# Kernel optimization log

Hardware: AMD Instinct MI355X
Metric: run time of the kernel (lower is better)

Reference implementation:

```python
import jax, jax.numpy as jnp
import numpy as np

N = 100000      # nodes
IN_DIM = 128    # input feature dim
HID = 64        # hidden_dim / out_dim per head
HEADS = 4
E_RAND = 1600000  # random edges; self-loops appended -> E = E_RAND + N
SCALES = 3


def setup_inputs() -> dict:
    key = jax.random.key(0)
    ks = jax.random.split(key, 12)
    h = jax.random.normal(ks[0], (N, IN_DIM), dtype=jnp.float32)
    src = jax.random.randint(ks[1], (E_RAND,), 0, N)
    dst = jax.random.randint(ks[2], (E_RAND,), 0, N)
    loop = jnp.arange(N)
    src = jnp.concatenate([src, loop])  # self-loops ensure every dst has a mailbox
    dst = jnp.concatenate([dst, loop])
    frac_cover_mat = jax.random.randint(ks[3], (N, SCALES), 0, N)
    # learned params (bias=False everywhere); xavier-ish scaling
    layer1_fc = jax.random.normal(ks[4], (HEADS, HID, IN_DIM), jnp.float32) / np.sqrt(IN_DIM)
    layer1_attn = jax.random.normal(ks[5], (HEADS, 2 * HID), jnp.float32) * 0.1
    layer2_fc = jax.random.normal(ks[6], (HID, HID * HEADS), jnp.float32) / np.sqrt(HID * HEADS)
    layer2_attn = jax.random.normal(ks[7], (2 * HID,), jnp.float32) * 0.1
    frac_w = jax.random.normal(ks[8], (SCALES, HID, IN_DIM), jnp.float32) / np.sqrt(IN_DIM)
    frac_final_w = jax.random.normal(ks[9], (HID, SCALES * HID), jnp.float32) / np.sqrt(SCALES * HID)
    fc2_w = jax.random.normal(ks[10], (HID, 2 * HID), jnp.float32) / np.sqrt(2 * HID)
    return {"h": h, "src": src, "dst": dst, "frac_cover_mat": frac_cover_mat,
            "layer1_fc": layer1_fc, "layer1_attn": layer1_attn,
            "layer2_fc": layer2_fc, "layer2_attn": layer2_attn,
            "frac_w": frac_w, "frac_final_w": frac_final_w, "fc2_w": fc2_w}


def _gat_layer(z, src, dst, attn_w, n):
    # attn(cat([z_src, z_dst])) == z_src @ a_src + z_dst @ a_dst  (bias-free Linear)
    d = z.shape[1]
    e = jax.nn.leaky_relu(z[src] @ attn_w[:d] + z[dst] @ attn_w[d:])  # [E]
    # segment softmax over incoming edges of each dst node
    m = jax.ops.segment_max(e, dst, num_segments=n)
    ex = jnp.exp(e - m[dst])
    denom = jax.ops.segment_sum(ex, dst, num_segments=n)
    alpha = ex / denom[dst]                                   # [E]
    return jax.ops.segment_sum(alpha[:, None] * z[src], dst, num_segments=n)  # [N, d]


def reference(h, src, dst, frac_cover_mat,
              layer1_fc, layer1_attn, layer2_fc, layer2_attn,
              frac_w, frac_final_w, fc2_w):
    n = h.shape[0]
    # layer1: multi-head GAT, merge='cat'
    heads = []
    for i in range(layer1_fc.shape[0]):
        z = h @ layer1_fc[i].T                                # [N, HID]
        heads.append(_gat_layer(z, src, dst, layer1_attn[i], n))
    h_nei = jax.nn.elu(jnp.concatenate(heads, axis=1))        # [N, HID*HEADS]
    # layer2: single-head GAT
    z2 = h_nei @ layer2_fc.T                                  # [N, HID]
    h_nei = _gat_layer(z2, src, dst, layer2_attn, n)          # [N, HID]
    # fractal layer (dropout = identity in eval)
    h_all = [h[frac_cover_mat[:, s]] @ frac_w[s].T for s in range(frac_w.shape[0])]
    h_frac = jnp.concatenate(h_all, axis=1) @ frac_final_w.T  # [N, HID]
    # fc2 on cat([h_nei, h_frac]); dropout identity
    h_global = jnp.concatenate([h_nei, h_frac], axis=1) @ fc2_w.T  # [N, HID]
    # AvgPooling over single graph -> [1, HID]
    return jnp.mean(h_global, axis=0, keepdims=True)
```

## Files before the change

kernel.cpp:

```cpp
#include <hip/hip_runtime.h>
#include <math.h>


#define CAP 128

typedef unsigned int  uint_t;
typedef unsigned short ushort_t;
typedef __attribute__((ext_vector_type(8))) short short8;
typedef __attribute__((ext_vector_type(4))) float floatx4;
typedef __attribute__((ext_vector_type(2))) float floatx2;

__device__ __forceinline__ float wred_sum(float v){
#pragma unroll
  for (int o = 1; o < 64; o <<= 1) v += __shfl_xor(v, o, 64);
  return v;
}
__device__ __forceinline__ float lrelu(float x){ return x >= 0.f ? x : 0.01f*x; }
__device__ __forceinline__ ushort_t f2b(float f){
  uint_t u = __float_as_uint(f);
  u = (u + 0x7FFFu + ((u >> 16) & 1u)) >> 16;
  return (ushort_t)u;
}
__device__ __forceinline__ float b2f_lo(uint_t w){ return __uint_as_float(w << 16); }
__device__ __forceinline__ float b2f_hi(uint_t w){ return __uint_as_float(w & 0xFFFF0000u); }

__device__ __forceinline__ void agg8(uint2 u, float4 al,
    floatx2& c00, floatx2& c01, floatx2& c10, floatx2& c11){
  floatx2 p0 = __builtin_amdgcn_cvt_pk_f32_fp8(u.x, false);
  floatx2 p1 = __builtin_amdgcn_cvt_pk_f32_fp8(u.x, true);
  floatx2 p2 = __builtin_amdgcn_cvt_pk_f32_fp8(u.y, false);
  floatx2 p3 = __builtin_amdgcn_cvt_pk_f32_fp8(u.y, true);
  floatx2 aXY = {al.x, al.y}, aZW = {al.z, al.w};
  c00 += aXY * p0;
  c01 += aZW * p1;
  c10 += aXY * p2;
  c11 += aZW * p3;
}

__global__ void k_prep(const float* __restrict__ W1, const float* __restrict__ W2,
                       const float* __restrict__ a1, const float* __restrict__ a2,
                       const int* __restrict__ dstI, int E,
                       const int* __restrict__ fcm, int N3, int* __restrict__ cnt,
                       ushort_t* __restrict__ w1bp, float* __restrict__ v2,
                       int* __restrict__ deg){
  __shared__ float v[8][128];
  const int bx = blockIdx.x, t = threadIdx.x;
  if (bx < 128){
    int idx = bx*256 + t;
    int j = idx & 7, lane = (idx >> 3) & 63, ks = (idx >> 9) & 3, tt = idx >> 11;
    int n = tt*16 + (lane & 15), k = ks*32 + (lane >> 4)*8 + j;
    int hh = tt >> 2, m = tt & 3;
    int pt = (m < 2) ? (hh*2 + m) : (8 + hh*2 + (m - 2));
    w1bp[((pt*4 + ks)*64 + lane)*8 + j] = f2b(W1[n*128 + k]);
  } else if (bx == 128){
    for (int o = t; o < 1024; o += 256){
      int col = o >> 7, k = o & 127, hh = col & 3, off = (col >> 2)*64;
      float s = 0.f;
      for (int n = 0; n < 64; n++) s += a1[hh*128 + off + n] * W1[(hh*64 + n)*128 + k];
      v[col][k] = s;
    }
    __syncthreads();
    for (int idx = t; idx < 2048; idx += 256){
      int j = idx & 7, lane = (idx >> 3) & 63, ks = idx >> 9;
      int col = lane & 15, k = ks*32 + (lane >> 4)*8 + j;
      w1bp[32768 + idx] = (col < 8) ? f2b(v[col][k]) : (ushort_t)0;
    }
  } else if (bx == 129){
    float s0 = 0.f, s1 = 0.f;
    for (int j = 0; j < 64; j++){
      float wjk = W2[j*256 + t];
      s0 += wjk * a2[j];
      s1 += wjk * a2[64 + j];
    }
    v2[t] = s0; v2[256 + t] = s1;
  } else {
    const int nb = gridDim.x - 130;
    for (int i = (bx-130)*256 + t; i < E; i += nb*256)
      atomicAdd(&deg[dstI[i]], 1);
    for (int i = (bx-130)*256 + t; i < N3; i += nb*256){
      int v3 = fcm[i];
      atomicAdd(&cnt[v3*3 + (i % 3)], 1);
    }
  }
}

__global__ __launch_bounds__(256) void k_scan1(const int* __restrict__ deg, int* __restrict__ part){
  __shared__ int tmp[256];
  int t = threadIdx.x;
  tmp[t] = deg[blockIdx.x*256 + t];
  __syncthreads();
  for (int off = 128; off > 0; off >>= 1){
    if (t < off) tmp[t] += tmp[t+off];
    __syncthreads();
  }
  if (t == 0) part[blockIdx.x] = tmp[0];
}
__global__ __launch_bounds__(512) void k_scan2(int* __restrict__ part, int B){
  __shared__ int tmp[512];
  int t = threadIdx.x;
  int v = (t < B) ? part[t] : 0;
  tmp[t] = v; __syncthreads();
  for (int off = 1; off < 512; off <<= 1){
    int x = (t >= off) ? tmp[t-off] : 0;
    __syncthreads();
    tmp[t] += x;
    __syncthreads();
  }
  if (t < B) part[t] = tmp[t] - v;
}
__global__ __launch_bounds__(256) void k_scan3(const int* __restrict__ deg, const int* __restrict__ part,
    int* __restrict__ rowptr, int* __restrict__ cursor){
  __shared__ int tmp[256];
  int t = threadIdx.x, i = blockIdx.x*256 + t;
  int v = deg[i];
  tmp[t] = v; __syncthreads();
  for (int off = 1; off < 256; off <<= 1){
    int x = (t >= off) ? tmp[t-off] : 0;
    __syncthreads();
    tmp[t] += x;
    __syncthreads();
  }
  int excl = tmp[t] - v + part[blockIdx.x];
  rowptr[i] = excl; cursor[i] = excl;
}

__global__ __launch_bounds__(512, 4) void k_mega(const float* __restrict__ h,
    const ushort_t* __restrict__ w1bp,
    uint_t* __restrict__ z8, float* __restrict__ s1s, float* __restrict__ s1d, int N,
    const int* __restrict__ srcI, const int* __restrict__ dstI,
    int* __restrict__ cursor, int* __restrict__ csr, int E,
    int Gg, int Gs, int G, int step,
    const int* __restrict__ cnt, float* __restrict__ accFrac)
{
  static __shared__ __align__(16) char smem[36864];
  const int tid = threadIdx.x;
  const int id = (int)(((unsigned long long)blockIdx.x * (unsigned)step) % (unsigned)G);
  if (id < Gg){
    ushort_t* ldsB = (ushort_t*)smem;
    const int wave = tid >> 6, lane = tid & 63;
    const int quad = lane >> 4, l16 = lane & 15;
    const int row0 = id*128 + wave*16;
    const bool act = row0 < N;
    const int ar = act ? ((row0 + l16 < N) ? (row0 + l16) : (N - 1)) : 0;
    short8 AHI[4], ALO[4];
    if (act){
#pragma unroll
      for (int ks = 0; ks < 4; ks++){
        const float* ap = &h[(size_t)ar*128 + ks*32 + quad*8];
        float4 v0 = *(const float4*)ap;
        float4 v1 = *(const float4*)(ap + 4);
        float vv[8] = {v0.x,v0.y,v0.z,v0.w,v1.x,v1.y,v1.z,v1.w};
#pragma unroll
        for (int j = 0; j < 8; j++){
          ushort_t hb = f2b(vv[j]);
          float hf = __uint_as_float((uint_t)hb << 16);
          AHI[ks][j] = (short)hb;
          ALO[ks][j] = (short)f2b(vv[j] - hf);
        }
      }
    }
#pragma unroll
    for (int half = 0; half < 2; half++){
      __syncthreads();
      {
        const int cnt4 = half ? 2304 : 2048;
        const uint4* src = (const uint4*)w1bp + (half ? 2048 : 0);
        uint4* dst = (uint4*)ldsB;
        for (int i = tid; i < cnt4; i += 512) dst[i] = src[i];
      }
      __syncthreads();
      if (!act) continue;
      const int nt = half ? 9 : 8;
      floatx4 c[9];
#pragma unroll
      for (int i = 0; i < 9; i++) c[i] = (floatx4){0.f,0.f,0.f,0.f};
#pragma unroll
      for (int ks = 0; ks < 4; ks++){
        for (int i = 0; i < nt; i++){
          short8 b = *(const short8*)&ldsB[(size_t)((i*4 + ks)*64 + lane)*8];
          c[i] = __builtin_amdgcn_mfma_f32_16x16x32_bf16(AHI[ks], b, c[i], 0, 0, 0);
        }
        if (half){
          short8 b = *(const short8*)&ldsB[(size_t)((8*4 + ks)*64 + lane)*8];
          c[8] = __builtin_amdgcn_mfma_f32_16x16x32_bf16(ALO[ks], b, c[8], 0, 0, 0);
        }
      }
      const int m0 = half ? 2 : 0;
#pragma unroll
      for (int i = 0; i < 4; i++){
        const int r = row0 + quad*4 + i;
        if (r >= N) continue;
#pragma unroll
        for (int dm = 0; dm < 2; dm++){
          int u = 0;
          u = __builtin_amdgcn_cvt_pk_fp8_f32(c[0*2+dm][i], c[1*2+dm][i], u, false);
          u = __builtin_amdgcn_cvt_pk_fp8_f32(c[2*2+dm][i], c[3*2+dm][i], u, true);
          z8[(size_t)r*64 + (m0+dm)*16 + l16] = (uint_t)u;
        }
        if (half){
          const float sv = c[8][i];
          if (l16 < 4) s1s[r*4 + l16] = sv;
          else if (l16 < 8) s1d[r*4 + (l16 - 4)] = sv;
        }
      }
    }
  } else if (id < Gg + Gs){
    const int i = (id - Gg)*512 + tid;
    if (i < E){
      int p = atomicAdd(&cursor[dstI[i]], 1);
      csr[p] = srcI[i];
    }
  } else {
    float (*red)[384] = (float(*)[384])smem;
    const int wave = tid >> 6, lane = tid & 63;
    const int g = lane >> 5, li = lane & 31;
    const int Gf = G - Gg - Gs;
    const int stream0 = (id - Gg - Gs)*16 + wave*2 + g;
    const int step16 = Gf * 16;
    float4 a0 = {0,0,0,0}, a1 = {0,0,0,0}, a2 = {0,0,0,0};
    for (int n = stream0; n < N; n += step16){
      const float w0 = (float)cnt[n*3];
      const float w1 = (float)cnt[n*3+1];
      const float w2 = (float)cnt[n*3+2];
      float4 v = *(const float4*)&h[(size_t)n*128 + li*4];
      a0.x += w0*v.x; a0.y += w0*v.y; a0.z += w0*v.z; a0.w += w0*v.w;
      a1.x += w1*v.x; a1.y += w1*v.y; a1.z += w1*v.z; a1.w += w1*v.w;
      a2.x += w2*v.x; a2.y += w2*v.y; a2.z += w2*v.z; a2.w += w2*v.w;
    }
    const int w16 = wave*2 + g;
    *(float4*)&red[w16][0*128 + li*4] = a0;
    *(float4*)&red[w16][1*128 + li*4] = a1;
    *(float4*)&red[w16][2*128 + li*4] = a2;
    __syncthreads();
    for (int i = tid; i < 384; i += 512){
      float v = 0.f;
#pragma unroll
      for (int w = 0; w < 16; w++) v += red[w][i];
      atomicAdd(&accFrac[i], v);
    }
  }
}

__global__ __launch_bounds__(256) void k_gat1(
    const uint_t* __restrict__ z8, const float* __restrict__ s1src, const float* __restrict__ s1dst,
    const int* __restrict__ rowptr, const int* __restrict__ csr, const float* __restrict__ v2,
    uint_t* __restrict__ hneib, float* __restrict__ s2s, float* __restrict__ s2d, int N)
{
  __shared__ int   sbuf[4][CAP];
  __shared__ __align__(16) float4 ebuf[4][CAP];
  __shared__ float v2s[512];
  const int tid = threadIdx.x;
  v2s[tid] = v2[tid];
  v2s[tid + 256] = v2[tid + 256];
  __syncthreads();
  const int wave = tid >> 6, lane = tid & 63;
  const int dst = blockIdx.x*4 + wave;
  if (dst >= N) return;
  const int beg = rowptr[dst];
  const int deg = rowptr[dst+1] - beg;
  const float4 sd = *(const float4*)&s1dst[dst*4];
  float t0=0.f,t1=0.f,t2=0.f,t3=0.f;
  for (int j = lane; j < deg; j += 64){
    int s = csr[beg+j];
    float4 sv = *(const float4*)&s1src[s*4];
    float4 a;
    a.x = __expf(lrelu(sv.x+sd.x)); a.y = __expf(lrelu(sv.y+sd.y));
    a.z = __expf(lrelu(sv.z+sd.z)); a.w = __expf(lrelu(sv.w+sd.w));
    if (j < CAP){ sbuf[wave][j] = s*64; ebuf[wave][j] = a; }
    t0 += a.x; t1 += a.y; t2 += a.z; t3 += a.w;
  }
  const float inv[4] = {1.f/wred_sum(t0), 1.f/wred_sum(t1), 1.f/wred_sum(t2), 1.f/wred_sum(t3)};
  const int eh = lane >> 5, li = lane & 31;
  floatx2 c00 = {0.f,0.f}, c01 = {0.f,0.f}, c10 = {0.f,0.f}, c11 = {0.f,0.f};
  if (deg <= CAP){
    const int j0 = (eh < deg) ? eh : 0;
    int offc = sbuf[wave][j0];
    float4 alc = ebuf[wave][j0];
    uint2 uc = *((const uint2*)(z8 + offc) + li);
    for (int jj = 0; jj + 2 <= deg; jj += 2){
      const int jn = jj + 2 + eh;
      const int jnc = (jn < deg) ? jn : (jj + eh);
      const int offn = sbuf[wave][jnc];
      const float4 aln = ebuf[wave][jnc];
      const uint2 un = *((const uint2*)(z8 + offn) + li);
      agg8(uc, alc, c00, c01, c10, c11);
      uc = un; alc = aln;
    }
    if ((deg & 1) && eh == 0)
      agg8(uc, alc, c00, c01, c10, c11);
  } else {
    for (int jj = 0; jj < deg; jj += 2){
      const int j = jj + eh;
      const bool v = j < deg;
      const int jc = v ? j : jj;
      int off; float4 al;
      if (jc < CAP){ off = sbuf[wave][jc]; al = ebuf[wave][jc]; }
      else {
        int s = csr[beg+jc];
        off = s*64;
        float4 sv = *(const float4*)&s1src[s*4];
        al.x = __expf(lrelu(sv.x+sd.x)); al.y = __expf(lrelu(sv.y+sd.y));
        al.z = __expf(lrelu(sv.z+sd.z)); al.w = __expf(lrelu(sv.w+sd.w));
      }
      if (!v){ al.x=0.f; al.y=0.f; al.z=0.f; al.w=0.f; }
      uint2 u = *((const uint2*)(z8 + off) + li);
      agg8(u, al, c00, c01, c10, c11);
    }
  }
  float acc[2][4] = {{c00.x, c00.y, c01.x, c01.y},
                     {c10.x, c10.y, c11.x, c11.y}};
#pragma unroll
  for (int k = 0; k < 2; k++)
#pragma unroll
    for (int hh = 0; hh < 4; hh++) acc[k][hh] += __shfl_xor(acc[k][hh], 32, 64);
  const float* vv = &v2s[eh*256];
  float p = 0.f;
#pragma unroll
  for (int hh = 0; hh < 4; hh++){
    float e0 = acc[0][hh]*inv[hh]; e0 = e0 > 0.f ? e0 : expm1f(e0);
    float e1 = acc[1][hh]*inv[hh]; e1 = e1 > 0.f ? e1 : expm1f(e1);
    p += e0 * vv[hh*64 + 2*li] + e1 * vv[hh*64 + 2*li + 1];
    if ((hh >> 1) == eh)
      hneib[(size_t)dst*128 + hh*32 + li] = (uint_t)f2b(e0) | ((uint_t)f2b(e1) << 16);
  }
#pragma unroll
  for (int o = 1; o < 32; o <<= 1) p += __shfl_xor(p, o, 64);
  if (lane == 0)  s2s[dst] = p;
  if (lane == 32) s2d[dst] = p;
}

__global__ __launch_bounds__(256) void k_aw2(
    const float* __restrict__ s2s, const float* __restrict__ s2d,
    const int* __restrict__ rowptr, const int* __restrict__ csr,
    float* __restrict__ wsrc, int N)
{
  __shared__ int   sbuf[4][CAP];
  __shared__ float ebuf[4][CAP];
  const int wave = threadIdx.x >> 6, lane = threadIdx.x & 63;
  const int dst = blockIdx.x*4 + wave;
  if (dst >= N) return;
  const int beg = rowptr[dst], deg = rowptr[dst+1] - beg;
  const float sd = s2d[dst];
  float ts = 0.f;
  for (int j = lane; j < deg; j += 64){
    int s = csr[beg+j];
    float a = __expf(lrelu(s2s[s] + sd));
    if (j < CAP){ sbuf[wave][j] = s; ebuf[wave][j] = a; }
    ts += a;
  }
  const float inv = 1.f/wred_sum(ts);
  for (int j = lane; j < deg; j += 64){
    int s; float a;
    if (j < CAP){ s = sbuf[wave][j]; a = ebuf[wave][j]; }
    else { s = csr[beg+j]; a = __expf(lrelu(s2s[s] + sd)); }
    atomicAdd(&wsrc[s], a * inv);
  }
}

__global__ __launch_bounds__(256) void k_hsum(const uint_t* __restrict__ hneib,
    const float* __restrict__ wsrc, float* __restrict__ acc256, int N)
{
  __shared__ float pr[512];
  const int t = threadIdx.x;
  const int h2 = t >> 7, p = t & 127;
  float a0 = 0.f, a1 = 0.f;
  const int step = gridDim.x * 2;
  for (int n = blockIdx.x*2 + h2; n < N; n += step){
    float wn = wsrc[n];
    uint_t u = hneib[(size_t)n*128 + p];
    a0 += wn * b2f_lo(u);
    a1 += wn * b2f_hi(u);
  }
  pr[h2*256 + 2*p]     = a0;
  pr[h2*256 + 2*p + 1] = a1;
  __syncthreads();
  float v = pr[t] + pr[256 + t];
  int pp = t >> 1;
  int d = (pp >> 5)*64 + 2*(pp & 31) + (t & 1);
  atomicAdd(&acc256[d], v);
}

__global__ __launch_bounds__(256) void k_finalize(const float* __restrict__ acc256,
    const float* __restrict__ accFrac, const float* __restrict__ W2,
    const float* __restrict__ frw, const float* __restrict__ frf,
    const float* __restrict__ fc2, float* __restrict__ out, float invN)
{
  __shared__ float mh[256], nei[64], g[384], mm[192], hfrac[64];
  int t = threadIdx.x;
  mh[t] = acc256[t] * invN;
  for (int i = t; i < 384; i += 256) g[i] = accFrac[i] * invN;
  __syncthreads();
  if (t < 64){
    float s = 0.f;
    for (int k = 0; k < 256; k++) s += W2[t*256 + k] * mh[k];
    nei[t] = s;
  }
  for (int i = t; i < 192; i += 256){
    int s = i >> 6, d = i & 63;
    const float* w = frw + (size_t)(s*64 + d)*128;
    const float* gs = g + s*128;
    float sum = 0.f;
    for (int k = 0; k < 128; k++) sum += gs[k]*w[k];
    mm[i] = sum;
  }
  __syncthreads();
  if (t < 64){
    float s = 0.f;
    for (int k = 0; k < 192; k++) s += mm[k]*frf[t*192 + k];
    hfrac[t] = s;
  }
  __syncthreads();
  if (t < 64){
    float o = 0.f;
    for (int k = 0; k < 64; k++)
      o += fc2[t*128 + k]*nei[k] + fc2[t*128 + 64 + k]*hfrac[k];
    out[t] = o;
  }
}

extern "C" void kernel_launch(void* const* d_in, const int* in_sizes, int n_in,
                              void* d_out, int out_size, void* d_ws, size_t ws_size,
                              hipStream_t stream)
{
  const float* h    = (const float*)d_in[0];
  const int*   srcI = (const int*)  d_in[1];
  const int*   dstI = (const int*)  d_in[2];
  const int*   fcm  = (const int*)  d_in[3];
  const float* l1fc = (const float*)d_in[4];
  const float* l1at = (const float*)d_in[5];
  const float* l2fc = (const float*)d_in[6];
  const float* l2at = (const float*)d_in[7];
  const float* frw  = (const float*)d_in[8];
  const float* frf  = (const float*)d_in[9];
  const float* fc2  = (const float*)d_in[10];
  float* out = (float*)d_out;
  (void)n_in; (void)out_size; (void)ws_size;

  const int N = in_sizes[0] / 128;
  const int E = in_sizes[1];
  const int B = (N + 256) / 256;
  const int PAD = B * 256;

  char* w = (char*)d_ws;
  size_t off = 0;
  auto alloc = [&](size_t bytes) -> char* {
    char* p = w + off; off = (off + bytes + 255) & ~(size_t)255; return p;
  };
  uint_t* z8    = (uint_t*)alloc((size_t)N*64*4);
  uint_t* hneib = (uint_t*)alloc((size_t)N*128*4);
  float* s1s  = (float*)alloc((size_t)N*4*4);
  float* s1d  = (float*)alloc((size_t)N*4*4);
  float* s2s  = (float*)alloc((size_t)N*4);
  float* s2d  = (float*)alloc((size_t)N*4);
  int*   deg     = (int*)  alloc((size_t)PAD*4);
  int*   cnt     = (int*)  alloc((size_t)N*3*4);
  float* wsrc    = (float*)alloc((size_t)N*4);
  float* acc256  = (float*)alloc(256*4);
  float* accFrac = (float*)alloc(384*4);
  const size_t zbytes = (size_t)((char*)accFrac + 384*4 - (char*)deg);
  int*   rowptr = (int*)alloc((size_t)PAD*4);
  int*   cursor = (int*)alloc((size_t)PAD*4);
  int*   part   = (int*)alloc(512*4);
  int*   csr    = (int*)alloc((size_t)E*4);
  ushort_t* w1bp = (ushort_t*)alloc(34816*2);
  float* v2     = (float*)alloc(512*4);

  hipMemsetAsync(deg, 0, zbytes, stream);

  hipLaunchKernelGGL(k_prep,  dim3(130 + 512), dim3(256), 0, stream,
                     l1fc, l2fc, l1at, l2at, dstI, E, fcm, 3*N, cnt, w1bp, v2, deg);
  hipLaunchKernelGGL(k_scan1, dim3(B),   dim3(256), 0, stream, deg, part);
  hipLaunchKernelGGL(k_scan2, dim3(1),   dim3(512), 0, stream, part, B);
  hipLaunchKernelGGL(k_scan3, dim3(B),   dim3(256), 0, stream, deg, part, rowptr, cursor);

  const int Gg = (N + 127) / 128;
  const int Gs = (E + 511) / 512;
  const int Gf = 512;
  const int G  = Gg + Gs + Gf;
  int step = (int)(G * 0.618) | 1;
  auto gcd = [](int a, int b){ while (b){ int t = a % b; a = b; b = t; } return a; };
  while (gcd(step, G) != 1) step += 2;

  hipLaunchKernelGGL(k_mega,  dim3(G), dim3(512), 0, stream,
                     h, w1bp, z8, s1s, s1d, N,
                     srcI, dstI, cursor, csr, E, Gg, Gs, G, step,
                     cnt, accFrac);
  hipLaunchKernelGGL(k_gat1,  dim3((N+3)/4), dim3(256), 0, stream,
                     z8, s1s, s1d, rowptr, csr, v2, hneib, s2s, s2d, N);
  hipLaunchKernelGGL(k_aw2,   dim3((N+3)/4), dim3(256), 0, stream,
                     s2s, s2d, rowptr, csr, wsrc, N);
  hipLaunchKernelGGL(k_hsum,  dim3(608),     dim3(256), 0, stream,
                     hneib, wsrc, acc256, N);
  hipLaunchKernelGGL(k_finalize, dim3(1),    dim3(256), 0, stream,
                     acc256, accFrac, l2fc, frw, frf, fc2, out, 1.0f/(float)N);
}
```

Before: 526.9 us.

## Split layer-1 GAT aggregation across feature halves with four edge groups per wave

The layer-1 GAT kernel launches twice as many blocks, and each block handles one half of the feature columns for a set of destination nodes. Each wave now processes four edges at a time in 16-lane groups instead of two edges in 32-lane groups, and the software-prefetch loop is replaced by one generic loop. Because each half produces only a partial layer-2 score, s2s and s2d are now accumulated with atomics. Those buffers move into the memset-zeroed region so the partials start from zero. This aims to raise parallelism and memory-level concurrency for the gather, at the cost of computing the softmax weights twice per edge, loading the CSR and score arrays twice, and adding atomics.

```diff
diff --git a/kernel.cpp b/kernel.cpp
--- a/kernel.cpp
+++ b/kernel.cpp
@@ -244,7 +244,7 @@
 __global__ __launch_bounds__(256) void k_gat1(
     const uint_t* __restrict__ z8, const float* __restrict__ s1src, const float* __restrict__ s1dst,
     const int* __restrict__ rowptr, const int* __restrict__ csr, const float* __restrict__ v2,
-    uint_t* __restrict__ hneib, float* __restrict__ s2s, float* __restrict__ s2d, int N)
+    uint_t* __restrict__ hneib, float* __restrict__ s2s, float* __restrict__ s2d, int N, int nb)
 {
   __shared__ int   sbuf[4][CAP];
   __shared__ __align__(16) float4 ebuf[4][CAP];
@@ -253,11 +253,14 @@
   v2s[tid] = v2[tid];
   v2s[tid + 256] = v2[tid + 256];
   __syncthreads();
+  const int h0 = (blockIdx.x >= nb) ? 1 : 0;
+  const int bx = blockIdx.x - (h0 ? nb : 0);
   const int wave = tid >> 6, lane = tid & 63;
-  const int dst = blockIdx.x*4 + wave;
+  const int dst = bx*4 + wave;
   if (dst >= N) return;
   const int beg = rowptr[dst];
   const int deg = rowptr[dst+1] - beg;
+  const int hoff = h0*32;
   const float4 sd = *(const float4*)&s1dst[dst*4];
   float t0=0.f,t1=0.f,t2=0.f,t3=0.f;
   for (int j = lane; j < deg; j += 64){
@@ -266,67 +269,55 @@
     float4 a;
     a.x = __expf(lrelu(sv.x+sd.x)); a.y = __expf(lrelu(sv.y+sd.y));
     a.z = __expf(lrelu(sv.z+sd.z)); a.w = __expf(lrelu(sv.w+sd.w));
-    if (j < CAP){ sbuf[wave][j] = s*64; ebuf[wave][j] = a; }
+    if (j < CAP){ sbuf[wave][j] = s*64 + hoff; ebuf[wave][j] = a; }
     t0 += a.x; t1 += a.y; t2 += a.z; t3 += a.w;
   }
   const float inv[4] = {1.f/wred_sum(t0), 1.f/wred_sum(t1), 1.f/wred_sum(t2), 1.f/wred_sum(t3)};
-  const int eh = lane >> 5, li = lane & 31;
+  const int sg = lane >> 4, li = lane & 15;
   floatx2 c00 = {0.f,0.f}, c01 = {0.f,0.f}, c10 = {0.f,0.f}, c11 = {0.f,0.f};
-  if (deg <= CAP){
-    const int j0 = (eh < deg) ? eh : 0;
-    int offc = sbuf[wave][j0];
-    float4 alc = ebuf[wave][j0];
-    uint2 uc = *((const uint2*)(z8 + offc) + li);
-    for (int jj = 0; jj + 2 <= deg; jj += 2){
-      const int jn = jj + 2 + eh;
-      const int jnc = (jn < deg) ? jn : (jj + eh);
-      const int offn = sbuf[wave][jnc];
-      const float4 aln = ebuf[wave][jnc];
-      const uint2 un = *((const uint2*)(z8 + offn) + li);
-      agg8(uc, alc, c00, c01, c10, c11);
-      uc = un; alc = aln;
-    }
-    if ((deg & 1) && eh == 0)
-      agg8(uc, alc, c00, c01, c10, c11);
-  } else {
-    for (int jj = 0; jj < deg; jj += 2){
-      const int j = jj + eh;
-      const bool v = j < deg;
-      const int jc = v ? j : jj;
-      int off; float4 al;
-      if (jc < CAP){ off = sbuf[wave][jc]; al = ebuf[wave][jc]; }
-      else {
-        int s = csr[beg+jc];
-        off = s*64;
-        float4 sv = *(const float4*)&s1src[s*4];
-        al.x = __expf(lrelu(sv.x+sd.x)); al.y = __expf(lrelu(sv.y+sd.y));
-        al.z = __expf(lrelu(sv.z+sd.z)); al.w = __expf(lrelu(sv.w+sd.w));
-      }
-      if (!v){ al.x=0.f; al.y=0.f; al.z=0.f; al.w=0.f; }
-      uint2 u = *((const uint2*)(z8 + off) + li);
-      agg8(u, al, c00, c01, c10, c11);
-    }
-  }
-  float acc[2][4] = {{c00.x, c00.y, c01.x, c01.y},
-                     {c10.x, c10.y, c11.x, c11.y}};
-#pragma unroll
-  for (int k = 0; k < 2; k++)
-#pragma unroll
-    for (int hh = 0; hh < 4; hh++) acc[k][hh] += __shfl_xor(acc[k][hh], 32, 64);
-  const float* vv = &v2s[eh*256];
-  float p = 0.f;
-#pragma unroll
-  for (int hh = 0; hh < 4; hh++){
-    float e0 = acc[0][hh]*inv[hh]; e0 = e0 > 0.f ? e0 : expm1f(e0);
-    float e1 = acc[1][hh]*inv[hh]; e1 = e1 > 0.f ? e1 : expm1f(e1);
-    p += e0 * vv[hh*64 + 2*li] + e1 * vv[hh*64 + 2*li + 1];
-    if ((hh >> 1) == eh)
-      hneib[(size_t)dst*128 + hh*32 + li] = (uint_t)f2b(e0) | ((uint_t)f2b(e1) << 16);
-  }
-#pragma unroll
-  for (int o = 1; o < 32; o <<= 1) p += __shfl_xor(p, o, 64);
-  if (lane == 0)  s2s[dst] = p;
-  if (lane == 32) s2d[dst] = p;
+  for (int jj = 0; jj < deg; jj += 4){
+    const int j = jj + sg;
+    const bool valid = j < deg;
+    const int jc = valid ? j : jj;
+    int off; float4 al;
+    if (jc < CAP){ off = sbuf[wave][jc]; al = ebuf[wave][jc]; }
+    else {
+      int s = csr[beg+jc];
+      off = s*64 + hoff;
+      float4 sv = *(const float4*)&s1src[s*4];
+      al.x = __expf(lrelu(sv.x+sd.x)); al.y = __expf(lrelu(sv.y+sd.y));
+      al.z = __expf(lrelu(sv.z+sd.z)); al.w = __expf(lrelu(sv.w+sd.w));
+    }
+    if (!valid){ al.x=0.f; al.y=0.f; al.z=0.f; al.w=0.f; }
+    uint2 u = *((const uint2*)(z8 + off) + li);
+    agg8(u, al, c00, c01, c10, c11);
+  }
+  float e[8] = {c00.x, c00.y, c01.x, c01.y,
+                c10.x, c10.y, c11.x, c11.y};
+#pragma unroll
+  for (int q = 0; q < 8; q++){
+    e[q] += __shfl_xor(e[q], 16, 64);
+    e[q] += __shfl_xor(e[q], 32, 64);
+  }
+  const int ce = hoff + 2*li;
+  float ps = 0.f, pd = 0.f;
+  uint_t wsel = 0;
+#pragma unroll
+  for (int q = 0; q < 4; q++){
+    float e0 = e[q]   * inv[q]; e0 = e0 > 0.f ? e0 : expm1f(e0);
+    float e1 = e[4+q] * inv[q]; e1 = e1 > 0.f ? e1 : expm1f(e1);
+    ps += e0 * v2s[q*64 + ce]       + e1 * v2s[q*64 + ce + 1];
+    pd += e0 * v2s[256 + q*64 + ce] + e1 * v2s[256 + q*64 + ce + 1];
+    uint_t w = (uint_t)f2b(e0) | ((uint_t)f2b(e1) << 16);
+    if (q == sg) wsel = w;
+  }
+  hneib[(size_t)dst*128 + sg*32 + h0*16 + li] = wsel;
+  ps = wred_sum(ps) * 0.25f;
+  pd = wred_sum(pd) * 0.25f;
+  if (lane == 0){
+    atomicAdd(&s2s[dst], ps);
+    atomicAdd(&s2d[dst], pd);
+  }
 }
 
 __global__ __launch_bounds__(256) void k_aw2(
@@ -450,11 +441,11 @@
   uint_t* hneib = (uint_t*)alloc((size_t)N*128*4);
   float* s1s  = (float*)alloc((size_t)N*4*4);
   float* s1d  = (float*)alloc((size_t)N*4*4);
-  float* s2s  = (float*)alloc((size_t)N*4);
-  float* s2d  = (float*)alloc((size_t)N*4);
   int*   deg     = (int*)  alloc((size_t)PAD*4);
   int*   cnt     = (int*)  alloc((size_t)N*3*4);
   float* wsrc    = (float*)alloc((size_t)N*4);
+  float* s2s     = (float*)alloc((size_t)N*4);
+  float* s2d     = (float*)alloc((size_t)N*4);
   float* acc256  = (float*)alloc(256*4);
   float* accFrac = (float*)alloc(384*4);
   const size_t zbytes = (size_t)((char*)accFrac + 384*4 - (char*)deg);
@@ -485,12 +476,13 @@
                      h, w1bp, z8, s1s, s1d, N,
                      srcI, dstI, cursor, csr, E, Gg, Gs, G, step,
                      cnt, accFrac);
-  hipLaunchKernelGGL(k_gat1,  dim3((N+3)/4), dim3(256), 0, stream,
-                     z8, s1s, s1d, rowptr, csr, v2, hneib, s2s, s2d, N);
-  hipLaunchKernelGGL(k_aw2,   dim3((N+3)/4), dim3(256), 0, stream,
+  const int nb = (N + 3) / 4;
+  hipLaunchKernelGGL(k_gat1,  dim3(2*nb), dim3(256), 0, stream,
+                     z8, s1s, s1d, rowptr, csr, v2, hneib, s2s, s2d, N, nb);
+  hipLaunchKernelGGL(k_aw2,   dim3(nb),   dim3(256), 0, stream,
                      s2s, s2d, rowptr, csr, wsrc, N);
-  hipLaunchKernelGGL(k_hsum,  dim3(608),     dim3(256), 0, stream,
+  hipLaunchKernelGGL(k_hsum,  dim3(608),  dim3(256), 0, stream,
                      hneib, wsrc, acc256, N);
-  hipLaunchKernelGGL(k_finalize, dim3(1),    dim3(256), 0, stream,
+  hipLaunchKernelGGL(k_finalize, dim3(1), dim3(256), 0, stream,
                      acc256, accFrac, l2fc, frw, frf, fc2, out, 1.0f/(float)N);
 }
```

Result: slower. 598.4 us (+13.6%).

## Privatize degree and weight atomics per XCD with workgroup-scope atomics

Applied to the files above, without the earlier changes.

Degree counting and the layer-2 source-weight scatter now go to eight per-XCD private arrays, indexed by the hardware XCC id, using relaxed workgroup-scope atomics. The CSR fill no longer needs a second atomic cursor pass: each edge records its rank within its XCD slice during counting, and the scan produces per-XCD base offsets. The aim is to cut device-scope atomic traffic and cross-die coherence cost. In exchange, the memset covers larger zeroed buffers and the readers must sum eight slices. Workgroup-scope atomics on global memory rely on all blocks of one XCD sharing an L2, which may be unsafe on this hardware.

```diff
diff --git a/kernel.cpp b/kernel.cpp
--- a/kernel.cpp
+++ b/kernel.cpp
@@ -10,6 +10,11 @@
 typedef __attribute__((ext_vector_type(4))) float floatx4;
 typedef __attribute__((ext_vector_type(2))) float floatx2;
 
+__device__ __forceinline__ unsigned xcc_id(){
+  unsigned x;
+  asm volatile("s_getreg_b32 %0, hwreg(HW_REG_XCC_ID)" : "=s"(x));
+  return x & 7u;
+}
 __device__ __forceinline__ float wred_sum(float v){
 #pragma unroll
   for (int o = 1; o < 64; o <<= 1) v += __shfl_xor(v, o, 64);
@@ -42,7 +47,7 @@
                        const int* __restrict__ dstI, int E,
                        const int* __restrict__ fcm, int N3, int* __restrict__ cnt,
                        ushort_t* __restrict__ w1bp, float* __restrict__ v2,
-                       int* __restrict__ deg){
+                       int* __restrict__ deg8, int* __restrict__ rk, int PAD){
   __shared__ float v[8][128];
   const int bx = blockIdx.x, t = threadIdx.x;
   if (bx < 128){
@@ -75,8 +80,14 @@
     v2[t] = s0; v2[256 + t] = s1;
   } else {
     const int nb = gridDim.x - 130;
-    for (int i = (bx-130)*256 + t; i < E; i += nb*256)
-      atomicAdd(&deg[dstI[i]], 1);
+    const unsigned xcd = xcc_id();
+    int* myDeg = deg8 + (size_t)xcd * PAD;
+    for (int i = (bx-130)*256 + t; i < E; i += nb*256){
+      int d = dstI[i];
+      int r = __hip_atomic_fetch_add(&myDeg[d], 1, __ATOMIC_RELAXED,
+                                     __HIP_MEMORY_SCOPE_WORKGROUP);
+      rk[i] = (int)((xcd << 28) | (unsigned)r);
+    }
     for (int i = (bx-130)*256 + t; i < N3; i += nb*256){
       int v3 = fcm[i];
       atomicAdd(&cnt[v3*3 + (i % 3)], 1);
@@ -84,10 +95,14 @@
   }
 }
 
-__global__ __launch_bounds__(256) void k_scan1(const int* __restrict__ deg, int* __restrict__ part){
+__global__ __launch_bounds__(256) void k_scan1(const int* __restrict__ deg8,
+    int* __restrict__ part, int PAD){
   __shared__ int tmp[256];
-  int t = threadIdx.x;
-  tmp[t] = deg[blockIdx.x*256 + t];
+  int t = threadIdx.x, i = blockIdx.x*256 + t;
+  int v = 0;
+#pragma unroll
+  for (int x = 0; x < 8; x++) v += deg8[(size_t)x*PAD + i];
+  tmp[t] = v;
   __syncthreads();
   for (int off = 128; off > 0; off >>= 1){
     if (t < off) tmp[t] += tmp[t+off];
@@ -108,11 +123,14 @@
   }
   if (t < B) part[t] = tmp[t] - v;
 }
-__global__ __launch_bounds__(256) void k_scan3(const int* __restrict__ deg, const int* __restrict__ part,
-    int* __restrict__ rowptr, int* __restrict__ cursor){
+__global__ __launch_bounds__(256) void k_scan3(const int* __restrict__ deg8,
+    const int* __restrict__ part, int* __restrict__ rowptr,
+    int* __restrict__ base8, int PAD){
   __shared__ int tmp[256];
   int t = threadIdx.x, i = blockIdx.x*256 + t;
-  int v = deg[i];
+  int d8[8]; int v = 0;
+#pragma unroll
+  for (int x = 0; x < 8; x++){ d8[x] = deg8[(size_t)x*PAD + i]; v += d8[x]; }
   tmp[t] = v; __syncthreads();
   for (int off = 1; off < 256; off <<= 1){
     int x = (t >= off) ? tmp[t-off] : 0;
@@ -121,14 +139,18 @@
     __syncthreads();
   }
   int excl = tmp[t] - v + part[blockIdx.x];
-  rowptr[i] = excl; cursor[i] = excl;
+  rowptr[i] = excl;
+  int run = excl;
+#pragma unroll
+  for (int x = 0; x < 8; x++){ base8[(size_t)x*PAD + i] = run; run += d8[x]; }
 }
 
 __global__ __launch_bounds__(512, 4) void k_mega(const float* __restrict__ h,
     const ushort_t* __restrict__ w1bp,
     uint_t* __restrict__ z8, float* __restrict__ s1s, float* __restrict__ s1d, int N,
     const int* __restrict__ srcI, const int* __restrict__ dstI,
-    int* __restrict__ cursor, int* __restrict__ csr, int E,
+    const int* __restrict__ rk, const int* __restrict__ base8, int PAD,
+    int* __restrict__ csr, int E,
     int Gg, int Gs, int G, int step,
     const int* __restrict__ cnt, float* __restrict__ accFrac)
 {
@@ -207,7 +229,9 @@
   } else if (id < Gg + Gs){
     const int i = (id - Gg)*512 + tid;
     if (i < E){
-      int p = atomicAdd(&cursor[dstI[i]], 1);
+      const int d = dstI[i];
+      const uint_t u = (uint_t)rk[i];
+      const int p = base8[(size_t)(u >> 28)*PAD + d] + (int)(u & 0x0FFFFFFFu);
       csr[p] = srcI[i];
     }
   } else {
@@ -332,10 +356,12 @@
 __global__ __launch_bounds__(256) void k_aw2(
     const float* __restrict__ s2s, const float* __restrict__ s2d,
     const int* __restrict__ rowptr, const int* __restrict__ csr,
-    float* __restrict__ wsrc, int N)
+    float* __restrict__ wsrc8, int N)
 {
   __shared__ int   sbuf[4][CAP];
   __shared__ float ebuf[4][CAP];
+  const unsigned xcd = xcc_id();
+  float* ws = wsrc8 + (size_t)xcd * N;
   const int wave = threadIdx.x >> 6, lane = threadIdx.x & 63;
   const int dst = blockIdx.x*4 + wave;
   if (dst >= N) return;
@@ -353,12 +379,13 @@
     int s; float a;
     if (j < CAP){ s = sbuf[wave][j]; a = ebuf[wave][j]; }
     else { s = csr[beg+j]; a = __expf(lrelu(s2s[s] + sd)); }
-    atomicAdd(&wsrc[s], a * inv);
+    __hip_atomic_fetch_add(&ws[s], a * inv, __ATOMIC_RELAXED,
+                           __HIP_MEMORY_SCOPE_WORKGROUP);
   }
 }
 
 __global__ __launch_bounds__(256) void k_hsum(const uint_t* __restrict__ hneib,
-    const float* __restrict__ wsrc, float* __restrict__ acc256, int N)
+    const float* __restrict__ wsrc8, float* __restrict__ acc256, int N)
 {
   __shared__ float pr[512];
   const int t = threadIdx.x;
@@ -366,7 +393,9 @@
   float a0 = 0.f, a1 = 0.f;
   const int step = gridDim.x * 2;
   for (int n = blockIdx.x*2 + h2; n < N; n += step){
-    float wn = wsrc[n];
+    float wn = 0.f;
+#pragma unroll
+    for (int x = 0; x < 8; x++) wn += wsrc8[(size_t)x*N + n];
     uint_t u = hneib[(size_t)n*128 + p];
     a0 += wn * b2f_lo(u);
     a1 += wn * b2f_hi(u);
@@ -448,30 +477,33 @@
   };
   uint_t* z8    = (uint_t*)alloc((size_t)N*64*4);
   uint_t* hneib = (uint_t*)alloc((size_t)N*128*4);
+  int*    rk    = (int*)hneib;
   float* s1s  = (float*)alloc((size_t)N*4*4);
   float* s1d  = (float*)alloc((size_t)N*4*4);
   float* s2s  = (float*)alloc((size_t)N*4);
   float* s2d  = (float*)alloc((size_t)N*4);
-  int*   deg     = (int*)  alloc((size_t)PAD*4);
+  int*   deg8    = (int*)  alloc((size_t)8*PAD*4);
   int*   cnt     = (int*)  alloc((size_t)N*3*4);
-  float* wsrc    = (float*)alloc((size_t)N*4);
+  float* wsrc8   = (float*)alloc((size_t)8*N*4);
   float* acc256  = (float*)alloc(256*4);
   float* accFrac = (float*)alloc(384*4);
-  const size_t zbytes = (size_t)((char*)accFrac + 384*4 - (char*)deg);
+  const size_t zbytes = (size_t)((char*)accFrac + 384*4 - (char*)deg8);
   int*   rowptr = (int*)alloc((size_t)PAD*4);
-  int*   cursor = (int*)alloc((size_t)PAD*4);
+  int*   base8  = (int*)alloc((size_t)8*PAD*4);
   int*   part   = (int*)alloc(512*4);
   int*   csr    = (int*)alloc((size_t)E*4);
   ushort_t* w1bp = (ushort_t*)alloc(34816*2);
   float* v2     = (float*)alloc(512*4);
 
-  hipMemsetAsync(deg, 0, zbytes, stream);
+  hipMemsetAsync(deg8, 0, zbytes, stream);
 
   hipLaunchKernelGGL(k_prep,  dim3(130 + 512), dim3(256), 0, stream,
-                     l1fc, l2fc, l1at, l2at, dstI, E, fcm, 3*N, cnt, w1bp, v2, deg);
-  hipLaunchKernelGGL(k_scan1, dim3(B),   dim3(256), 0, stream, deg, part);
+                     l1fc, l2fc, l1at, l2at, dstI, E, fcm, 3*N, cnt, w1bp, v2,
+                     deg8, rk, PAD);
+  hipLaunchKernelGGL(k_scan1, dim3(B),   dim3(256), 0, stream, deg8, part, PAD);
   hipLaunchKernelGGL(k_scan2, dim3(1),   dim3(512), 0, stream, part, B);
-  hipLaunchKernelGGL(k_scan3, dim3(B),   dim3(256), 0, stream, deg, part, rowptr, cursor);
+  hipLaunchKernelGGL(k_scan3, dim3(B),   dim3(256), 0, stream, deg8, part,
+                     rowptr, base8, PAD);
 
   const int Gg = (N + 127) / 128;
   const int Gs = (E + 511) / 512;
@@ -483,14 +515,14 @@
 
   hipLaunchKernelGGL(k_mega,  dim3(G), dim3(512), 0, stream,
                      h, w1bp, z8, s1s, s1d, N,
-                     srcI, dstI, cursor, csr, E, Gg, Gs, G, step,
+                     srcI, dstI, rk, base8, PAD, csr, E, Gg, Gs, G, step,
                      cnt, accFrac);
   hipLaunchKernelGGL(k_gat1,  dim3((N+3)/4), dim3(256), 0, stream,
                      z8, s1s, s1d, rowptr, csr, v2, hneib, s2s, s2d, N);
   hipLaunchKernelGGL(k_aw2,   dim3((N+3)/4), dim3(256), 0, stream,
-                     s2s, s2d, rowptr, csr, wsrc, N);
+                     s2s, s2d, rowptr, csr, wsrc8, N);
   hipLaunchKernelGGL(k_hsum,  dim3(608),     dim3(256), 0, stream,
-                     hneib, wsrc, acc256, N);
+                     hneib, wsrc8, acc256, N);
   hipLaunchKernelGGL(k_finalize, dim3(1),    dim3(256), 0, stream,
                      acc256, accFrac, l2fc, frw, frf, fc2, out, 1.0f/(float)N);
 }
```

Result: faster. 514.5 us, median of 2 (-2.4%).
